# Optimization experiments

Hardware: AMD Instinct MI355X
Metric: run time of the kernel (lower is better)

The kernel has to match this reference:

```python
import jax, jax.numpy as jnp
import numpy as np

N_CELLS = 1024
HID = 256
IN_DIM = 256
OUT_DIM = 256
NOISE_DIM = 32
N_LOOP = 32  # min(32, n_cells)


def _lin(x, W, b):
    # torch nn.Linear: y = x @ W.T + b, W shape [out, in]
    return x @ W.T + b


def faction_sync_debate(h, step, n_factions=8, sync=0.15, debate=0.15):
    n, d = h.shape
    n_f = min(n_factions, n // 2)
    if n_f < 2:
        return h
    fs = n // n_f  # assumes n_f * fs == n (true for 1024/8)
    blk = h.reshape(n_f, fs, d)
    # per-faction mean pull (disjoint slices -> order independent)
    blk = (1.0 - sync) * blk + sync * blk.mean(axis=1, keepdims=True)
    if step > 5:  # step is a Python int -> static branch
        global_opinion = blk.mean(axis=1).mean(axis=0)  # [d]
        dc = max(1, fs // 4)
        blk = blk.at[:, :dc, :].set((1.0 - debate) * blk[:, :dc, :] + debate * global_opinion)
    return blk.reshape(n, d)


def setup_inputs() -> dict:
    key = jax.random.key(0)
    ks = iter(jax.random.split(key, 32))

    def rn(shape, scale=0.02):
        return (jax.random.normal(next(ks), shape, dtype=jnp.float32) * scale)

    flat = N_CELLS * HID  # 262144
    inp = {
        "x": rn((1, IN_DIM), 1.0),
        "noise": rn((1, NOISE_DIM), 1.0),
        "cell_hiddens": rn((N_CELLS, HID), 0.1),
        # generator: Linear(in+32,256) -> ReLU -> Linear(256,512) -> ReLU -> Linear(512, flat)
        "gen_W1": rn((256, IN_DIM + NOISE_DIM)), "gen_b1": rn((256,)),
        "gen_W2": rn((512, 256)), "gen_b2": rn((512,)),
        "gen_W3": rn((flat, 512)), "gen_b3": rn((flat,)),
        # discriminator: Linear(flat,512) -> LReLU(0.2) -> Linear(512,256) -> LReLU -> Linear(256,1) -> Sigmoid
        "disc_W1": rn((512, flat)), "disc_b1": rn((512,)),
        "disc_W2": rn((256, 512)), "disc_b2": rn((256,)),
        "disc_W3": rn((1, 256)), "disc_b3": rn((1,)),
        # mind engines: Linear(in+hid,128) -> ReLU -> Linear(128,out)
        "ea_W1": rn((128, IN_DIM + HID)), "ea_b1": rn((128,)),
        "ea_W2": rn((OUT_DIM, 128)), "ea_b2": rn((OUT_DIM,)),
        "eg_W1": rn((128, IN_DIM + HID)), "eg_b1": rn((128,)),
        "eg_W2": rn((OUT_DIM, 128)), "eg_b2": rn((OUT_DIM,)),
        # GRUCell(out+1, hid): gate order r, z, n
        "gru_Wih": rn((3 * HID, OUT_DIM + 1)), "gru_bih": rn((3 * HID,)),
        "gru_Whh": rn((3 * HID, HID)), "gru_bhh": rn((3 * HID,)),
        "step": 10,
    }
    return inp


def reference(x, noise, cell_hiddens,
              gen_W1, gen_b1, gen_W2, gen_b2, gen_W3, gen_b3,
              disc_W1, disc_b1, disc_W2, disc_b2, disc_W3, disc_b3,
              ea_W1, ea_b1, ea_W2, ea_b2, eg_W1, eg_b1, eg_W2, eg_b2,
              gru_Wih, gru_bih, gru_Whh, gru_bhh, step):
    sg = jax.lax.stop_gradient
    # --- generate_states ---
    gi = jnp.concatenate([x, noise], axis=-1)           # [1, in+32]
    h1 = jax.nn.relu(_lin(gi, gen_W1, gen_b1))
    h2 = jax.nn.relu(_lin(h1, gen_W2, gen_b2))
    gen_states = _lin(h2, gen_W3, gen_b3).reshape(N_CELLS, HID)
    # torch: gen_states.detach() then faction sync+debate
    synced = faction_sync_debate(sg(gen_states), step)
    # --- batched BenchMind over first 32 cells (replaces Python loop) ---
    H = synced[:N_LOOP]                                  # [32, HID]
    X = jnp.broadcast_to(x, (N_LOOP, x.shape[-1]))       # [32, IN]
    comb = jnp.concatenate([X, H], axis=-1)              # [32, IN+HID]
    a = _lin(jax.nn.relu(_lin(comb, ea_W1, ea_b1)), ea_W2, ea_b2)
    g = _lin(jax.nn.relu(_lin(comb, eg_W1, eg_b1)), eg_W2, eg_b2)
    outputs = a - g                                      # [32, OUT]
    tensions = (outputs ** 2).mean(axis=-1)              # [32]
    # GRUCell update (mem inputs detached as in torch)
    mem_in = jnp.concatenate([sg(outputs), sg(tensions)[:, None]], axis=-1)  # [32, OUT+1]
    gih = _lin(mem_in, gru_Wih, gru_bih)
    ghh = _lin(H, gru_Whh, gru_bhh)
    ir, iz, i_n = jnp.split(gih, 3, axis=-1)
    hr, hz, h_n = jnp.split(ghh, 3, axis=-1)
    r = jax.nn.sigmoid(ir + hr)
    z = jax.nn.sigmoid(iz + hz)
    n_cand = jnp.tanh(i_n + r * h_n)
    new_hiddens = (1.0 - z) * n_cand + z * H             # [32, HID]
    # --- buffer update (no_grad) + discriminate ---
    new_cell_hiddens = sg(0.7 * synced + 0.3 * cell_hiddens)

    def disc(s):
        f = s.reshape(1, -1)
        d1 = jax.nn.leaky_relu(_lin(f, disc_W1, disc_b1), 0.2)
        d2 = jax.nn.leaky_relu(_lin(d1, disc_W2, disc_b2), 0.2)
        return jax.nn.sigmoid(_lin(d2, disc_W3, disc_b3))

    d_real = disc(new_cell_hiddens)
    d_fake = disc(gen_states)
    # tensions were .item()'d in torch -> constants
    mean_tension = sg(tensions).mean()
    w = jax.nn.softmax(sg(tensions))                     # [32]
    combined = (w[:, None] * outputs).sum(axis=0, keepdims=True)  # [1, OUT]
    return combined, mean_tension, d_real, d_fake, new_hiddens
```

## Files before the change

kernel.cpp:

```cpp
#include <hip/hip_runtime.h>
#include <hip/hip_bf16.h>
#include <math.h>

#define N_CELLS 1024
#define HID     256
#define IN_DIM  256
#define NOISE_DIM 32
#define OUT_DIM 256
#define N_LOOP  32
#define FLAT    (N_CELLS*HID)

__device__ __forceinline__ float wave_reduce64(float v) {
    #pragma unroll
    for (int m = 32; m; m >>= 1) v += __shfl_xor(v, m);
    return v;
}
__device__ __forceinline__ float wave_reduce32(float v) {
    #pragma unroll
    for (int m = 16; m; m >>= 1) v += __shfl_xor(v, m);
    return v;
}

__global__ void k_gen_h1(const float* __restrict__ x, const float* __restrict__ noise,
                         const float* __restrict__ W1, const float* __restrict__ b1,
                         float* __restrict__ h1) {
    __shared__ __align__(16) float gi[288];
    int t = threadIdx.x, l = t & 63, w = t >> 6;
    gi[t] = x[t];
    if (t < 32) gi[256 + t] = noise[t];
    __syncthreads();
    int j = blockIdx.x * 4 + w;
    const float4* wr = (const float4*)(W1 + j * 288);
    const float4* g4 = (const float4*)gi;
    float4 a = wr[l], v = g4[l];
    float acc = a.x*v.x + a.y*v.y + a.z*v.z + a.w*v.w;
    if (l < 8) {
        float4 a2 = wr[64 + l], v2 = g4[64 + l];
        acc += a2.x*v2.x + a2.y*v2.y + a2.z*v2.z + a2.w*v2.w;
    }
    acc = wave_reduce64(acc);
    if (l == 0) h1[j] = fmaxf(acc + b1[j], 0.f);
}

__global__ void k_gen_h2(const float* __restrict__ h1, const float* __restrict__ W2,
                         const float* __restrict__ b2, float* __restrict__ h2) {
    int t = threadIdx.x, l = t & 63, w = t >> 6;
    int j = blockIdx.x * 4 + w;
    float4 a = ((const float4*)(W2 + j * 256))[l];
    float4 v = ((const float4*)h1)[l];
    float acc = a.x*v.x + a.y*v.y + a.z*v.z + a.w*v.w;
    acc = wave_reduce64(acc);
    if (l == 0) h2[j] = fmaxf(acc + b2[j], 0.f);
}

__global__ void k_gen_big(const float* __restrict__ W3, const float* __restrict__ b3,
                          const float* __restrict__ h2, float* __restrict__ gs) {
    int lane = threadIdx.x & 63;
    int row  = blockIdx.x * (blockDim.x >> 6) + (threadIdx.x >> 6);
    const float4* h24 = (const float4*)h2;
    float4 ha = h24[lane], hb = h24[64 + lane];
    const float4* w4 = (const float4*)(W3 + (size_t)row * 512);
    float4 wa = w4[lane], wb = w4[64 + lane];
    float acc = wa.x*ha.x + wa.y*ha.y + wa.z*ha.z + wa.w*ha.w
              + wb.x*hb.x + wb.y*hb.y + wb.z*hb.z + wb.w*hb.w;
    acc = wave_reduce64(acc);
    if (lane == 0) gs[row] = acc + b3[row];
}

__global__ void k_fmean(const float* __restrict__ gs, float* __restrict__ fmean) {
    __shared__ float part[4][64];
    int b = blockIdx.x, t = threadIdx.x;
    int f = b >> 2, q = b & 3;
    int c = q * 64 + (t & 63), rg = t >> 6;
    const float* base = gs + (size_t)(f * 128 + rg * 32) * 256 + c;
    float s = 0.f;
    for (int i = 0; i < 32; ++i) s += base[(size_t)i * 256];
    part[rg][t & 63] = s;
    __syncthreads();
    if (t < 64) {
        float v = part[0][t] + part[1][t] + part[2][t] + part[3][t];
        fmean[f * 256 + q * 64 + t] = v * (1.f / 128.f);
    }
}

__global__ void k_sync(const float* __restrict__ gs, const float* __restrict__ fmean,
                       const float* __restrict__ ch, const int* __restrict__ step,
                       const float* __restrict__ x,
                       float* __restrict__ synced, float* __restrict__ ncn,
                       float* __restrict__ comb) {
    int c = blockIdx.x, d = threadIdx.x;
    int f = c >> 7;
    float gm = 0.f;
    #pragma unroll
    for (int k = 0; k < 8; ++k) gm += fmean[k * 256 + d];
    gm *= 0.125f;
    float fm = fmean[f * 256 + d];
    float v = 0.85f * gs[c * 256 + d] + 0.15f * fm;
    if (((c & 127) < 32) && (*step > 5)) v = 0.85f * v + 0.15f * gm;
    synced[c * 256 + d] = v;
    ncn[c * 256 + d] = 0.7f * v + 0.3f * ch[c * 256 + d];
    if (c < N_LOOP) {
        comb[c * 512 + d] = x[d];
        comb[c * 512 + 256 + d] = v;
    }
}

__global__ void k_ev1(const float* __restrict__ comb,
                      const float* __restrict__ eaW1, const float* __restrict__ eab1,
                      const float* __restrict__ egW1, const float* __restrict__ egb1,
                      float* __restrict__ h1ag) {
    __shared__ __align__(16) float cl[N_LOOP * 512];
    int t = threadIdx.x, l = t & 63, w = t >> 6;
    const float4* cg = (const float4*)comb;
    float4* c4 = (float4*)cl;
    for (int i = t; i < N_LOOP * 128; i += 256) c4[i] = cg[i];
    __syncthreads();
    int j = blockIdx.x * 4 + w;
    const float* W = (j < 128) ? (eaW1 + j * 512) : (egW1 + (j - 128) * 512);
    float bias = (j < 128) ? eab1[j] : egb1[j - 128];
    const float4* w4 = (const float4*)W;
    float4 wa = w4[l], wb = w4[64 + l];
    for (int i = 0; i < N_LOOP; ++i) {
        const float4* ci = (const float4*)(cl + i * 512);
        float4 va = ci[l], vb = ci[64 + l];
        float acc = wa.x*va.x + wa.y*va.y + wa.z*va.z + wa.w*va.w
                  + wb.x*vb.x + wb.y*vb.y + wb.z*vb.z + wb.w*vb.w;
        acc = wave_reduce64(acc);
        if (l == 0) h1ag[i * 256 + j] = fmaxf(acc + bias, 0.f);
    }
}

__global__ void k_ev2(const float* __restrict__ h1ag,
                      const float* __restrict__ eaW2, const float* __restrict__ eab2,
                      const float* __restrict__ egW2, const float* __restrict__ egb2,
                      float* __restrict__ outputs) {
    __shared__ __align__(16) float hl[N_LOOP * 256];
    int t = threadIdx.x, l = t & 63, w = t >> 6;
    const float4* hg4 = (const float4*)h1ag;
    float4* h4 = (float4*)hl;
    for (int i = t; i < N_LOOP * 64; i += 256) h4[i] = hg4[i];
    __syncthreads();
    int half = l >> 5, sl = l & 31;
    int tr = (blockIdx.x * 4 + w) * 2 + half;
    float4 wa = ((const float4*)(eaW2 + tr * 128))[sl];
    float4 wg = ((const float4*)(egW2 + tr * 128))[sl];
    float bias = eab2[tr] - egb2[tr];
    for (int i = 0; i < N_LOOP; ++i) {
        float4 va = *(const float4*)(hl + i * 256 + sl * 4);
        float4 vg = *(const float4*)(hl + i * 256 + 128 + sl * 4);
        float acc = wa.x*va.x + wa.y*va.y + wa.z*va.z + wa.w*va.w
                  - (wg.x*vg.x + wg.y*vg.y + wg.z*vg.z + wg.w*vg.w);
        acc = wave_reduce32(acc);
        if (sl == 0) outputs[i * 256 + tr] = acc + bias;
    }
}

__global__ void k_tension(const float* __restrict__ outputs, float* __restrict__ tensions) {
    __shared__ float red[256];
    int i = blockIdx.x, t = threadIdx.x;
    float o = outputs[i * 256 + t];
    red[t] = o * o;
    __syncthreads();
    for (int m = 128; m; m >>= 1) { if (t < m) red[t] += red[t + m]; __syncthreads(); }
    if (t == 0) tensions[i] = red[0] * (1.f / 256.f);
}

__global__ void k_gru(const float* __restrict__ outputs, const float* __restrict__ tensions,
                      const float* __restrict__ synced,
                      const float* __restrict__ Wih, const float* __restrict__ bih,
                      const float* __restrict__ Whh, const float* __restrict__ bhh,
                      float* __restrict__ rz, float* __restrict__ inb, float* __restrict__ hnb) {
    __shared__ __align__(16) float outs[N_LOOP * 256];
    __shared__ __align__(16) float Hl[N_LOOP * 256];
    __shared__ float tl[N_LOOP];
    int t = threadIdx.x, l = t & 63, w = t >> 6;
    {
        const float4* o4 = (const float4*)outputs;
        const float4* s4 = (const float4*)synced;
        float4* od = (float4*)outs;
        float4* hd = (float4*)Hl;
        for (int i = t; i < N_LOOP * 64; i += 256) { od[i] = o4[i]; hd[i] = s4[i]; }
        if (t < N_LOOP) tl[t] = tensions[t];
    }
    __syncthreads();
    int u = blockIdx.x * 4 + w;
    const float* wr = Wih + (size_t)u * 257;
    float w0 = wr[4*l], w1 = wr[4*l+1], w2 = wr[4*l+2], w3 = wr[4*l+3];
    float wlast = wr[256];
    float4 wh = ((const float4*)(Whh + (size_t)u * 256))[l];
    float bg = bih[u], bh = bhh[u];
    bool isN = (u >= 512);
    for (int i = 0; i < N_LOOP; ++i) {
        const float* oi = outs + i * 256 + 4 * l;
        const float* hi = Hl + i * 256 + 4 * l;
        float ga = w0*oi[0] + w1*oi[1] + w2*oi[2] + w3*oi[3];
        float hh = wh.x*hi[0] + wh.y*hi[1] + wh.z*hi[2] + wh.w*hi[3];
        if (!isN) {
            float s = wave_reduce64(ga + hh);
            if (l == 0) rz[i * 512 + u] = s + bg + bh + wlast * tl[i];
        } else {
            float sg = wave_reduce64(ga);
            float sh = wave_reduce64(hh);
            if (l == 0) {
                inb[i * 256 + (u - 512)] = sg + bg + wlast * tl[i];
                hnb[i * 256 + (u - 512)] = sh + bh;
            }
        }
    }
}

__global__ void k_gru_fin(const float* __restrict__ rz, const float* __restrict__ inb,
                          const float* __restrict__ hnb, const float* __restrict__ synced,
                          float* __restrict__ out) {
    int i = blockIdx.x, d = threadIdx.x;
    float r = 1.f / (1.f + expf(-rz[i * 512 + d]));
    float z = 1.f / (1.f + expf(-rz[i * 512 + 256 + d]));
    float nc = tanhf(inb[i * 256 + d] + r * hnb[i * 256 + d]);
    float H = synced[i * 256 + d];
    out[259 + i * 256 + d] = (1.f - z) * nc + z * H;
}

__global__ void k_disc1(const float* __restrict__ W1, const float* __restrict__ b1,
                        const float* __restrict__ real, const float* __restrict__ fake,
                        float* __restrict__ d1r, float* __restrict__ d1f) {
    __shared__ float sR[1024];
    __shared__ float sF[1024];
    int row = blockIdx.x, t = threadIdx.x;
    const float4* w4 = (const float4*)(W1 + (size_t)row * FLAT);
    const float4* r4 = (const float4*)real;
    const float4* f4 = (const float4*)fake;
    float aR = 0.f, aF = 0.f;
    for (int i = t; i < FLAT / 4; i += 1024) {
        float4 w = w4[i], r = r4[i], f = f4[i];
        aR += w.x*r.x + w.y*r.y + w.z*r.z + w.w*r.w;
        aF += w.x*f.x + w.y*f.y + w.z*f.z + w.w*f.w;
    }
    sR[t] = aR; sF[t] = aF;
    __syncthreads();
    for (int m = 512; m; m >>= 1) {
        if (t < m) { sR[t] += sR[t + m]; sF[t] += sF[t + m]; }
        __syncthreads();
    }
    if (t == 0) { d1r[row] = sR[0] + b1[row]; d1f[row] = sF[0] + b1[row]; }
}

__global__ void k_disc_tail(const float* __restrict__ W2, const float* __restrict__ b2,
                            const float* __restrict__ W3, const float* __restrict__ b3,
                            const float* __restrict__ d1r, const float* __restrict__ d1f,
                            float* __restrict__ out) {
    __shared__ __align__(16) float lv[512];
    __shared__ float l2[256];
    __shared__ float red[256];
    int b = blockIdx.x, t = threadIdx.x;
    const float* d1 = b ? d1f : d1r;
    for (int j = t; j < 512; j += 256) { float v = d1[j]; lv[j] = v > 0.f ? v : 0.2f * v; }
    __syncthreads();
    {
        float acc = b2[t];
        const float4* wr = (const float4*)(W2 + t * 512);
        const float4* l4 = (const float4*)lv;
        for (int k = 0; k < 128; ++k) {
            float4 w = wr[k], v = l4[k];
            acc += w.x*v.x + w.y*v.y + w.z*v.z + w.w*v.w;
        }
        l2[t] = acc > 0.f ? acc : 0.2f * acc;
    }
    __syncthreads();
    red[t] = l2[t] * W3[t];
    __syncthreads();
    for (int m = 128; m; m >>= 1) { if (t < m) red[t] += red[t + m]; __syncthreads(); }
    if (t == 0) { float v = red[0] + b3[0]; out[257 + b] = 1.f / (1.f + expf(-v)); }
}

__global__ void k_combine(const float* __restrict__ outputs, const float* __restrict__ tensions,
                          float* __restrict__ out) {
    __shared__ float w[32];
    __shared__ float ts[32];
    int t = threadIdx.x;
    if (t < 32) ts[t] = tensions[t];
    __syncthreads();
    if (t == 0) {
        float mx = ts[0];
        for (int i = 1; i < 32; ++i) mx = fmaxf(mx, ts[i]);
        float s = 0.f, mean = 0.f;
        for (int i = 0; i < 32; ++i) { float e = expf(ts[i] - mx); w[i] = e; s += e; mean += ts[i]; }
        float inv = 1.f / s;
        for (int i = 0; i < 32; ++i) w[i] *= inv;
        out[256] = mean * (1.f / 32.f);
    }
    __syncthreads();
    float c = 0.f;
    for (int i = 0; i < 32; ++i) c += w[i] * outputs[i * 256 + t];
    out[t] = c;
}

extern "C" void kernel_launch(void* const* d_in, const int* in_sizes, int n_in,
                              void* d_out, int out_size, void* d_ws, size_t ws_size,
                              hipStream_t stream) {
    const float* x     = (const float*)d_in[0];
    const float* noise = (const float*)d_in[1];
    const float* ch    = (const float*)d_in[2];
    const float* gW1   = (const float*)d_in[3];
    const float* gb1   = (const float*)d_in[4];
    const float* gW2   = (const float*)d_in[5];
    const float* gb2   = (const float*)d_in[6];
    const float* gW3   = (const float*)d_in[7];
    const float* gb3   = (const float*)d_in[8];
    const float* dW1   = (const float*)d_in[9];
    const float* db1   = (const float*)d_in[10];
    const float* dW2   = (const float*)d_in[11];
    const float* db2   = (const float*)d_in[12];
    const float* dW3   = (const float*)d_in[13];
    const float* db3   = (const float*)d_in[14];
    const float* eaW1  = (const float*)d_in[15];
    const float* eab1  = (const float*)d_in[16];
    const float* eaW2  = (const float*)d_in[17];
    const float* eab2  = (const float*)d_in[18];
    const float* egW1  = (const float*)d_in[19];
    const float* egb1  = (const float*)d_in[20];
    const float* egW2  = (const float*)d_in[21];
    const float* egb2  = (const float*)d_in[22];
    const float* Wih   = (const float*)d_in[23];
    const float* bih   = (const float*)d_in[24];
    const float* Whh   = (const float*)d_in[25];
    const float* bhh   = (const float*)d_in[26];
    const int*   step  = (const int*)d_in[27];

    float* out = (float*)d_out;
    float* ws  = (float*)d_ws;
    float* h1buf    = ws;
    float* h2       = h1buf + 256;
    float* gs       = h2 + 512;
    float* fmean    = gs + 262144;
    float* synced   = fmean + 2048;
    float* ncn      = synced + 262144;
    float* comb     = ncn + 262144;
    float* h1ag     = comb + 16384;
    float* outputs  = h1ag + 8192;
    float* tensions = outputs + 8192;
    float* rz       = tensions + 32;
    float* inb      = rz + 16384;
    float* hnb      = inb + 8192;
    float* d1r      = hnb + 8192;
    float* d1f      = d1r + 512;

    k_gen_h1<<<64, 256, 0, stream>>>(x, noise, gW1, gb1, h1buf);
    k_gen_h2<<<128, 256, 0, stream>>>(h1buf, gW2, gb2, h2);
    k_gen_big<<<FLAT / 4, 256, 0, stream>>>(gW3, gb3, h2, gs);
    k_fmean<<<32, 256, 0, stream>>>(gs, fmean);
    k_sync<<<1024, 256, 0, stream>>>(gs, fmean, ch, step, x, synced, ncn, comb);
    k_ev1<<<64, 256, 0, stream>>>(comb, eaW1, eab1, egW1, egb1, h1ag);
    k_ev2<<<32, 256, 0, stream>>>(h1ag, eaW2, eab2, egW2, egb2, outputs);
    k_tension<<<32, 256, 0, stream>>>(outputs, tensions);
    k_gru<<<192, 256, 0, stream>>>(outputs, tensions, synced, Wih, bih, Whh, bhh, rz, inb, hnb);
    k_gru_fin<<<32, 256, 0, stream>>>(rz, inb, hnb, synced, out);
    k_disc1<<<512, 1024, 0, stream>>>(dW1, db1, ncn, gs, d1r, d1f);
    k_disc_tail<<<2, 256, 0, stream>>>(dW2, db2, dW3, db3, d1r, d1f, out);
    k_combine<<<1, 256, 0, stream>>>(outputs, tensions, out);
}
```

Before: 302.5 us.

## Fuse small post-generator stages into cooperative megakernel with grid syncs

Merges the generator head layers into one cooperative kernel, and fuses fmean, sync, both evaluator layers, tension, GRU, GRU finalisation and combine into a single cooperative kernel separated by grid-wide barriers. The goal is to remove many small kernel launches and their gaps, which dominate these tiny stages. It also rewrites the disc1 block reduction to use wave shuffles instead of a 1024-entry shared-memory tree. Shared-memory staging is dropped in favour of direct global/L2 reads, and the old kernels are kept as a fallback if the cooperative launch fails. Grid syncs carry their own cost and require all 512 blocks to be co-resident.

```diff
diff --git a/kernel.cpp b/kernel.cpp
--- a/kernel.cpp
+++ b/kernel.cpp
@@ -1,6 +1,8 @@
 #include <hip/hip_runtime.h>
-#include <hip/hip_bf16.h>
+#include <hip/hip_cooperative_groups.h>
 #include <math.h>
+
+namespace cg = cooperative_groups;
 
 #define N_CELLS 1024
 #define HID     256
@@ -21,36 +23,40 @@
     return v;
 }
 
-__global__ void k_gen_h1(const float* __restrict__ x, const float* __restrict__ noise,
-                         const float* __restrict__ W1, const float* __restrict__ b1,
-                         float* __restrict__ h1) {
+__global__ void __launch_bounds__(256)
+k_gen_head(const float* __restrict__ x, const float* __restrict__ noise,
+           const float* __restrict__ W1, const float* __restrict__ b1,
+           const float* __restrict__ W2, const float* __restrict__ b2,
+           float* __restrict__ h1, float* __restrict__ h2) {
+    cg::grid_group grid = cg::this_grid();
     __shared__ __align__(16) float gi[288];
     int t = threadIdx.x, l = t & 63, w = t >> 6;
-    gi[t] = x[t];
-    if (t < 32) gi[256 + t] = noise[t];
-    __syncthreads();
-    int j = blockIdx.x * 4 + w;
-    const float4* wr = (const float4*)(W1 + j * 288);
-    const float4* g4 = (const float4*)gi;
-    float4 a = wr[l], v = g4[l];
-    float acc = a.x*v.x + a.y*v.y + a.z*v.z + a.w*v.w;
-    if (l < 8) {
-        float4 a2 = wr[64 + l], v2 = g4[64 + l];
-        acc += a2.x*v2.x + a2.y*v2.y + a2.z*v2.z + a2.w*v2.w;
-    }
-    acc = wave_reduce64(acc);
-    if (l == 0) h1[j] = fmaxf(acc + b1[j], 0.f);
-}
-
-__global__ void k_gen_h2(const float* __restrict__ h1, const float* __restrict__ W2,
-                         const float* __restrict__ b2, float* __restrict__ h2) {
-    int t = threadIdx.x, l = t & 63, w = t >> 6;
-    int j = blockIdx.x * 4 + w;
-    float4 a = ((const float4*)(W2 + j * 256))[l];
-    float4 v = ((const float4*)h1)[l];
-    float acc = a.x*v.x + a.y*v.y + a.z*v.z + a.w*v.w;
-    acc = wave_reduce64(acc);
-    if (l == 0) h2[j] = fmaxf(acc + b2[j], 0.f);
+    int wid = blockIdx.x * 4 + w;
+    if (blockIdx.x < 64) {
+        gi[t] = x[t];
+        if (t < 32) gi[256 + t] = noise[t];
+        __syncthreads();
+        int j = wid;
+        const float4* wr = (const float4*)(W1 + j * 288);
+        const float4* g4 = (const float4*)gi;
+        float4 a = wr[l], v = g4[l];
+        float acc = a.x*v.x + a.y*v.y + a.z*v.z + a.w*v.w;
+        if (l < 8) {
+            float4 a2 = wr[64 + l], v2 = g4[64 + l];
+            acc += a2.x*v2.x + a2.y*v2.y + a2.z*v2.z + a2.w*v2.w;
+        }
+        acc = wave_reduce64(acc);
+        if (l == 0) h1[j] = fmaxf(acc + b1[j], 0.f);
+    }
+    grid.sync();
+    {
+        int j = wid;
+        float4 a = ((const float4*)(W2 + j * 256))[l];
+        float4 v = ((const float4*)h1)[l];
+        float acc = a.x*v.x + a.y*v.y + a.z*v.z + a.w*v.w;
+        acc = wave_reduce64(acc);
+        if (l == 0) h2[j] = fmaxf(acc + b2[j], 0.f);
+    }
 }
 
 __global__ void k_gen_big(const float* __restrict__ W3, const float* __restrict__ b3,
@@ -65,6 +71,248 @@
               + wb.x*hb.x + wb.y*hb.y + wb.z*hb.z + wb.w*hb.w;
     acc = wave_reduce64(acc);
     if (lane == 0) gs[row] = acc + b3[row];
+}
+
+__global__ void __launch_bounds__(256)
+k_mega(const float* __restrict__ gs, const float* __restrict__ ch,
+       const int* __restrict__ step, const float* __restrict__ x,
+       const float* __restrict__ eaW1, const float* __restrict__ eab1,
+       const float* __restrict__ eaW2, const float* __restrict__ eab2,
+       const float* __restrict__ egW1, const float* __restrict__ egb1,
+       const float* __restrict__ egW2, const float* __restrict__ egb2,
+       const float* __restrict__ Wih, const float* __restrict__ bih,
+       const float* __restrict__ Whh, const float* __restrict__ bhh,
+       float* __restrict__ fmean, float* __restrict__ synced,
+       float* __restrict__ ncn, float* __restrict__ comb,
+       float* __restrict__ h1ag, float* __restrict__ outputs,
+       float* __restrict__ tensions, float* __restrict__ rz,
+       float* __restrict__ inb, float* __restrict__ hnb,
+       float* __restrict__ out) {
+    cg::grid_group grid = cg::this_grid();
+    int b = blockIdx.x, t = threadIdx.x, l = t & 63, w = t >> 6;
+    __shared__ float s0[4][64];
+    __shared__ float red[256];
+    __shared__ float sw[32];
+    __shared__ float sts[32];
+
+    if (b < 32) {
+        int f = b >> 2, q = b & 3;
+        int c = q * 64 + l, rg = w;
+        const float* base = gs + (size_t)(f * 128 + rg * 32) * 256 + c;
+        float s = 0.f;
+        for (int i = 0; i < 32; ++i) s += base[(size_t)i * 256];
+        s0[rg][l] = s;
+        __syncthreads();
+        if (t < 64)
+            fmean[f * 256 + q * 64 + t] =
+                (s0[0][t] + s0[1][t] + s0[2][t] + s0[3][t]) * (1.f / 128.f);
+    }
+    grid.sync();
+
+    {
+        int d = t;
+        float gm = 0.f;
+        #pragma unroll
+        for (int k = 0; k < 8; ++k) gm += fmean[k * 256 + d];
+        gm *= 0.125f;
+        bool deb = (*step > 5);
+        #pragma unroll
+        for (int cc = 0; cc < 2; ++cc) {
+            int c = b * 2 + cc;
+            int f = c >> 7;
+            float fm = fmean[f * 256 + d];
+            float v = 0.85f * gs[c * 256 + d] + 0.15f * fm;
+            if (((c & 127) < 32) && deb) v = 0.85f * v + 0.15f * gm;
+            synced[c * 256 + d] = v;
+            ncn[c * 256 + d] = 0.7f * v + 0.3f * ch[c * 256 + d];
+            if (c < N_LOOP) { comb[c * 512 + d] = x[d]; comb[c * 512 + 256 + d] = v; }
+        }
+    }
+    grid.sync();
+
+    if (b < 64) {
+        int j = b * 4 + w;
+        const float* W = (j < 128) ? (eaW1 + j * 512) : (egW1 + (j - 128) * 512);
+        float bias = (j < 128) ? eab1[j] : egb1[j - 128];
+        const float4* w4 = (const float4*)W;
+        float4 wa = w4[l], wb = w4[64 + l];
+        for (int i = 0; i < N_LOOP; ++i) {
+            const float4* ci = (const float4*)(comb + i * 512);
+            float4 va = ci[l], vb = ci[64 + l];
+            float acc = wa.x*va.x + wa.y*va.y + wa.z*va.z + wa.w*va.w
+                      + wb.x*vb.x + wb.y*vb.y + wb.z*vb.z + wb.w*vb.w;
+            acc = wave_reduce64(acc);
+            if (l == 0) h1ag[i * 256 + j] = fmaxf(acc + bias, 0.f);
+        }
+    }
+    grid.sync();
+
+    if (b < 64) {
+        int tr = b * 4 + w;
+        bool lo = (l < 32);
+        int sl = l & 31;
+        float4 wv = lo ? ((const float4*)(eaW2 + tr * 128))[sl]
+                       : ((const float4*)(egW2 + tr * 128))[sl];
+        float bias = eab2[tr] - egb2[tr];
+        for (int i = 0; i < N_LOOP; ++i) {
+            const float* hrow = h1ag + i * 256 + (lo ? 0 : 128);
+            float4 v = *(const float4*)(hrow + sl * 4);
+            float d_ = wv.x*v.x + wv.y*v.y + wv.z*v.z + wv.w*v.w;
+            float acc = lo ? d_ : -d_;
+            acc = wave_reduce64(acc);
+            if (l == 0) outputs[i * 256 + tr] = acc + bias;
+        }
+    }
+    grid.sync();
+
+    if (b < 32) {
+        float o = outputs[b * 256 + t];
+        red[t] = o * o;
+        __syncthreads();
+        for (int m = 128; m; m >>= 1) { if (t < m) red[t] += red[t + m]; __syncthreads(); }
+        if (t == 0) tensions[b] = red[0] * (1.f / 256.f);
+    }
+    grid.sync();
+
+    if (b < 192) {
+        int u = b * 4 + w;
+        const float* wr = Wih + (size_t)u * 257;
+        float w0 = wr[4*l], w1 = wr[4*l+1], w2 = wr[4*l+2], w3 = wr[4*l+3];
+        float wlast = wr[256];
+        float4 wh = ((const float4*)(Whh + (size_t)u * 256))[l];
+        float bg = bih[u], bh = bhh[u];
+        bool isN = (u >= 512);
+        for (int i = 0; i < N_LOOP; ++i) {
+            const float* oi = outputs + i * 256 + 4 * l;
+            const float* hi = synced + i * 256 + 4 * l;
+            float ga = w0*oi[0] + w1*oi[1] + w2*oi[2] + w3*oi[3];
+            float hh = wh.x*hi[0] + wh.y*hi[1] + wh.z*hi[2] + wh.w*hi[3];
+            if (!isN) {
+                float s = wave_reduce64(ga + hh);
+                if (l == 0) rz[i * 512 + u] = s + bg + bh + wlast * tensions[i];
+            } else {
+                float sg2 = wave_reduce64(ga);
+                float sh  = wave_reduce64(hh);
+                if (l == 0) {
+                    inb[i * 256 + (u - 512)] = sg2 + bg + wlast * tensions[i];
+                    hnb[i * 256 + (u - 512)] = sh + bh;
+                }
+            }
+        }
+    }
+    grid.sync();
+
+    if (b < 32) {
+        int i = b, d = t;
+        float r = 1.f / (1.f + expf(-rz[i * 512 + d]));
+        float z = 1.f / (1.f + expf(-rz[i * 512 + 256 + d]));
+        float nc = tanhf(inb[i * 256 + d] + r * hnb[i * 256 + d]);
+        float H = synced[i * 256 + d];
+        out[259 + i * 256 + d] = (1.f - z) * nc + z * H;
+    } else if (b == 32) {
+        if (t < 32) sts[t] = tensions[t];
+        __syncthreads();
+        if (t == 0) {
+            float mx = sts[0];
+            for (int i2 = 1; i2 < 32; ++i2) mx = fmaxf(mx, sts[i2]);
+            float s = 0.f, mean = 0.f;
+            for (int i2 = 0; i2 < 32; ++i2) { float e = expf(sts[i2] - mx); sw[i2] = e; s += e; mean += sts[i2]; }
+            float inv = 1.f / s;
+            for (int i2 = 0; i2 < 32; ++i2) sw[i2] *= inv;
+            out[256] = mean * (1.f / 32.f);
+        }
+        __syncthreads();
+        float c = 0.f;
+        for (int i2 = 0; i2 < 32; ++i2) c += sw[i2] * outputs[i2 * 256 + t];
+        out[t] = c;
+    }
+}
+
+__global__ void k_disc1(const float* __restrict__ W1, const float* __restrict__ b1,
+                        const float* __restrict__ real, const float* __restrict__ fake,
+                        float* __restrict__ d1r, float* __restrict__ d1f) {
+    __shared__ float sR[16];
+    __shared__ float sF[16];
+    int row = blockIdx.x, t = threadIdx.x, l = t & 63, w = t >> 6;
+    const float4* w4 = (const float4*)(W1 + (size_t)row * FLAT);
+    const float4* r4 = (const float4*)real;
+    const float4* f4 = (const float4*)fake;
+    float aR = 0.f, aF = 0.f;
+    for (int i = t; i < FLAT / 4; i += 1024) {
+        float4 ww = w4[i], r = r4[i], f = f4[i];
+        aR += ww.x*r.x + ww.y*r.y + ww.z*r.z + ww.w*r.w;
+        aF += ww.x*f.x + ww.y*f.y + ww.z*f.z + ww.w*f.w;
+    }
+    aR = wave_reduce64(aR);
+    aF = wave_reduce64(aF);
+    if (l == 0) { sR[w] = aR; sF[w] = aF; }
+    __syncthreads();
+    if (t < 16) {
+        float r = sR[t], f = sF[t];
+        #pragma unroll
+        for (int m = 8; m; m >>= 1) { r += __shfl_xor(r, m); f += __shfl_xor(f, m); }
+        if (t == 0) { d1r[row] = r + b1[row]; d1f[row] = f + b1[row]; }
+    }
+}
+
+__global__ void k_disc_tail(const float* __restrict__ W2, const float* __restrict__ b2,
+                            const float* __restrict__ W3, const float* __restrict__ b3,
+                            const float* __restrict__ d1r, const float* __restrict__ d1f,
+                            float* __restrict__ out) {
+    __shared__ __align__(16) float lv[512];
+    __shared__ float l2[256];
+    __shared__ float red[256];
+    int b = blockIdx.x, t = threadIdx.x;
+    const float* d1 = b ? d1f : d1r;
+    for (int j = t; j < 512; j += 256) { float v = d1[j]; lv[j] = v > 0.f ? v : 0.2f * v; }
+    __syncthreads();
+    {
+        float acc = b2[t];
+        const float4* wr = (const float4*)(W2 + t * 512);
+        const float4* l4 = (const float4*)lv;
+        for (int k = 0; k < 128; ++k) {
+            float4 w = wr[k], v = l4[k];
+            acc += w.x*v.x + w.y*v.y + w.z*v.z + w.w*v.w;
+        }
+        l2[t] = acc > 0.f ? acc : 0.2f * acc;
+    }
+    __syncthreads();
+    red[t] = l2[t] * W3[t];
+    __syncthreads();
+    for (int m = 128; m; m >>= 1) { if (t < m) red[t] += red[t + m]; __syncthreads(); }
+    if (t == 0) { float v = red[0] + b3[0]; out[257 + b] = 1.f / (1.f + expf(-v)); }
+}
+
+__global__ void k_gen_h1(const float* __restrict__ x, const float* __restrict__ noise,
+                         const float* __restrict__ W1, const float* __restrict__ b1,
+                         float* __restrict__ h1) {
+    __shared__ __align__(16) float gi[288];
+    int t = threadIdx.x, l = t & 63, w = t >> 6;
+    gi[t] = x[t];
+    if (t < 32) gi[256 + t] = noise[t];
+    __syncthreads();
+    int j = blockIdx.x * 4 + w;
+    const float4* wr = (const float4*)(W1 + j * 288);
+    const float4* g4 = (const float4*)gi;
+    float4 a = wr[l], v = g4[l];
+    float acc = a.x*v.x + a.y*v.y + a.z*v.z + a.w*v.w;
+    if (l < 8) {
+        float4 a2 = wr[64 + l], v2 = g4[64 + l];
+        acc += a2.x*v2.x + a2.y*v2.y + a2.z*v2.z + a2.w*v2.w;
+    }
+    acc = wave_reduce64(acc);
+    if (l == 0) h1[j] = fmaxf(acc + b1[j], 0.f);
+}
+
+__global__ void k_gen_h2(const float* __restrict__ h1, const float* __restrict__ W2,
+                         const float* __restrict__ b2, float* __restrict__ h2) {
+    int t = threadIdx.x, l = t & 63, w = t >> 6;
+    int j = blockIdx.x * 4 + w;
+    float4 a = ((const float4*)(W2 + j * 256))[l];
+    float4 v = ((const float4*)h1)[l];
+    float acc = a.x*v.x + a.y*v.y + a.z*v.z + a.w*v.w;
+    acc = wave_reduce64(acc);
+    if (l == 0) h2[j] = fmaxf(acc + b2[j], 0.f);
 }
 
 __global__ void k_fmean(const float* __restrict__ gs, float* __restrict__ fmean) {
@@ -109,19 +357,14 @@
                       const float* __restrict__ eaW1, const float* __restrict__ eab1,
                       const float* __restrict__ egW1, const float* __restrict__ egb1,
                       float* __restrict__ h1ag) {
-    __shared__ __align__(16) float cl[N_LOOP * 512];
     int t = threadIdx.x, l = t & 63, w = t >> 6;
-    const float4* cg = (const float4*)comb;
-    float4* c4 = (float4*)cl;
-    for (int i = t; i < N_LOOP * 128; i += 256) c4[i] = cg[i];
-    __syncthreads();
     int j = blockIdx.x * 4 + w;
     const float* W = (j < 128) ? (eaW1 + j * 512) : (egW1 + (j - 128) * 512);
     float bias = (j < 128) ? eab1[j] : egb1[j - 128];
     const float4* w4 = (const float4*)W;
     float4 wa = w4[l], wb = w4[64 + l];
     for (int i = 0; i < N_LOOP; ++i) {
-        const float4* ci = (const float4*)(cl + i * 512);
+        const float4* ci = (const float4*)(comb + i * 512);
         float4 va = ci[l], vb = ci[64 + l];
         float acc = wa.x*va.x + wa.y*va.y + wa.z*va.z + wa.w*va.w
                   + wb.x*vb.x + wb.y*vb.y + wb.z*vb.z + wb.w*vb.w;
@@ -134,24 +377,20 @@
                       const float* __restrict__ eaW2, const float* __restrict__ eab2,
                       const float* __restrict__ egW2, const float* __restrict__ egb2,
                       float* __restrict__ outputs) {
-    __shared__ __align__(16) float hl[N_LOOP * 256];
     int t = threadIdx.x, l = t & 63, w = t >> 6;
-    const float4* hg4 = (const float4*)h1ag;
-    float4* h4 = (float4*)hl;
-    for (int i = t; i < N_LOOP * 64; i += 256) h4[i] = hg4[i];
-    __syncthreads();
-    int half = l >> 5, sl = l & 31;
-    int tr = (blockIdx.x * 4 + w) * 2 + half;
-    float4 wa = ((const float4*)(eaW2 + tr * 128))[sl];
-    float4 wg = ((const float4*)(egW2 + tr * 128))[sl];
+    int tr = blockIdx.x * 4 + w;
+    bool lo = (l < 32);
+    int sl = l & 31;
+    float4 wv = lo ? ((const float4*)(eaW2 + tr * 128))[sl]
+                   : ((const float4*)(egW2 + tr * 128))[sl];
     float bias = eab2[tr] - egb2[tr];
     for (int i = 0; i < N_LOOP; ++i) {
-        float4 va = *(const float4*)(hl + i * 256 + sl * 4);
-        float4 vg = *(const float4*)(hl + i * 256 + 128 + sl * 4);
-        float acc = wa.x*va.x + wa.y*va.y + wa.z*va.z + wa.w*va.w
-                  - (wg.x*vg.x + wg.y*vg.y + wg.z*vg.z + wg.w*vg.w);
-        acc = wave_reduce32(acc);
-        if (sl == 0) outputs[i * 256 + tr] = acc + bias;
+        const float* hrow = h1ag + i * 256 + (lo ? 0 : 128);
+        float4 v = *(const float4*)(hrow + sl * 4);
+        float d_ = wv.x*v.x + wv.y*v.y + wv.z*v.z + wv.w*v.w;
+        float acc = lo ? d_ : -d_;
+        acc = wave_reduce64(acc);
+        if (l == 0) outputs[i * 256 + tr] = acc + bias;
     }
 }
 
@@ -170,19 +409,7 @@
                       const float* __restrict__ Wih, const float* __restrict__ bih,
                       const float* __restrict__ Whh, const float* __restrict__ bhh,
                       float* __restrict__ rz, float* __restrict__ inb, float* __restrict__ hnb) {
-    __shared__ __align__(16) float outs[N_LOOP * 256];
-    __shared__ __align__(16) float Hl[N_LOOP * 256];
-    __shared__ float tl[N_LOOP];
     int t = threadIdx.x, l = t & 63, w = t >> 6;
-    {
-        const float4* o4 = (const float4*)outputs;
-        const float4* s4 = (const float4*)synced;
-        float4* od = (float4*)outs;
-        float4* hd = (float4*)Hl;
-        for (int i = t; i < N_LOOP * 64; i += 256) { od[i] = o4[i]; hd[i] = s4[i]; }
-        if (t < N_LOOP) tl[t] = tensions[t];
-    }
-    __syncthreads();
     int u = blockIdx.x * 4 + w;
     const float* wr = Wih + (size_t)u * 257;
     float w0 = wr[4*l], w1 = wr[4*l+1], w2 = wr[4*l+2], w3 = wr[4*l+3];
@@ -191,18 +418,18 @@
     float bg = bih[u], bh = bhh[u];
     bool isN = (u >= 512);
     for (int i = 0; i < N_LOOP; ++i) {
-        const float* oi = outs + i * 256 + 4 * l;
-        const float* hi = Hl + i * 256 + 4 * l;
+        const float* oi = outputs + i * 256 + 4 * l;
+        const float* hi = synced + i * 256 + 4 * l;
         float ga = w0*oi[0] + w1*oi[1] + w2*oi[2] + w3*oi[3];
         float hh = wh.x*hi[0] + wh.y*hi[1] + wh.z*hi[2] + wh.w*hi[3];
         if (!isN) {
             float s = wave_reduce64(ga + hh);
-            if (l == 0) rz[i * 512 + u] = s + bg + bh + wlast * tl[i];
+            if (l == 0) rz[i * 512 + u] = s + bg + bh + wlast * tensions[i];
         } else {
-            float sg = wave_reduce64(ga);
-            float sh = wave_reduce64(hh);
+            float sg2 = wave_reduce64(ga);
+            float sh  = wave_reduce64(hh);
             if (l == 0) {
-                inb[i * 256 + (u - 512)] = sg + bg + wlast * tl[i];
+                inb[i * 256 + (u - 512)] = sg2 + bg + wlast * tensions[i];
                 hnb[i * 256 + (u - 512)] = sh + bh;
             }
         }
@@ -218,58 +445,6 @@
     float nc = tanhf(inb[i * 256 + d] + r * hnb[i * 256 + d]);
     float H = synced[i * 256 + d];
     out[259 + i * 256 + d] = (1.f - z) * nc + z * H;
-}
-
-__global__ void k_disc1(const float* __restrict__ W1, const float* __restrict__ b1,
-                        const float* __restrict__ real, const float* __restrict__ fake,
-                        float* __restrict__ d1r, float* __restrict__ d1f) {
-    __shared__ float sR[1024];
-    __shared__ float sF[1024];
-    int row = blockIdx.x, t = threadIdx.x;
-    const float4* w4 = (const float4*)(W1 + (size_t)row * FLAT);
-    const float4* r4 = (const float4*)real;
-    const float4* f4 = (const float4*)fake;
-    float aR = 0.f, aF = 0.f;
-    for (int i = t; i < FLAT / 4; i += 1024) {
-        float4 w = w4[i], r = r4[i], f = f4[i];
-        aR += w.x*r.x + w.y*r.y + w.z*r.z + w.w*r.w;
-        aF += w.x*f.x + w.y*f.y + w.z*f.z + w.w*f.w;
-    }
-    sR[t] = aR; sF[t] = aF;
-    __syncthreads();
-    for (int m = 512; m; m >>= 1) {
-        if (t < m) { sR[t] += sR[t + m]; sF[t] += sF[t + m]; }
-        __syncthreads();
-    }
-    if (t == 0) { d1r[row] = sR[0] + b1[row]; d1f[row] = sF[0] + b1[row]; }
-}
-
-__global__ void k_disc_tail(const float* __restrict__ W2, const float* __restrict__ b2,
-                            const float* __restrict__ W3, const float* __restrict__ b3,
-                            const float* __restrict__ d1r, const float* __restrict__ d1f,
-                            float* __restrict__ out) {
-    __shared__ __align__(16) float lv[512];
-    __shared__ float l2[256];
-    __shared__ float red[256];
-    int b = blockIdx.x, t = threadIdx.x;
-    const float* d1 = b ? d1f : d1r;
-    for (int j = t; j < 512; j += 256) { float v = d1[j]; lv[j] = v > 0.f ? v : 0.2f * v; }
-    __syncthreads();
-    {
-        float acc = b2[t];
-        const float4* wr = (const float4*)(W2 + t * 512);
-        const float4* l4 = (const float4*)lv;
-        for (int k = 0; k < 128; ++k) {
-            float4 w = wr[k], v = l4[k];
-            acc += w.x*v.x + w.y*v.y + w.z*v.z + w.w*v.w;
-        }
-        l2[t] = acc > 0.f ? acc : 0.2f * acc;
-    }
-    __syncthreads();
-    red[t] = l2[t] * W3[t];
-    __syncthreads();
-    for (int m = 128; m; m >>= 1) { if (t < m) red[t] += red[t + m]; __syncthreads(); }
-    if (t == 0) { float v = red[0] + b3[0]; out[257 + b] = 1.f / (1.f + expf(-v)); }
 }
 
 __global__ void k_combine(const float* __restrict__ outputs, const float* __restrict__ tensions,
@@ -344,17 +519,41 @@
     float* d1r      = hnb + 8192;
     float* d1f      = d1r + 512;
 
-    k_gen_h1<<<64, 256, 0, stream>>>(x, noise, gW1, gb1, h1buf);
-    k_gen_h2<<<128, 256, 0, stream>>>(h1buf, gW2, gb2, h2);
+    {
+        void* a[] = {(void*)&x, (void*)&noise, (void*)&gW1, (void*)&gb1,
+                     (void*)&gW2, (void*)&gb2, (void*)&h1buf, (void*)&h2};
+        hipError_t e = hipLaunchCooperativeKernel((const void*)k_gen_head,
+                                                  dim3(128), dim3(256), a, 0, stream);
+        if (e != hipSuccess) {
+            k_gen_h1<<<64, 256, 0, stream>>>(x, noise, gW1, gb1, h1buf);
+            k_gen_h2<<<128, 256, 0, stream>>>(h1buf, gW2, gb2, h2);
+        }
+    }
+
     k_gen_big<<<FLAT / 4, 256, 0, stream>>>(gW3, gb3, h2, gs);
-    k_fmean<<<32, 256, 0, stream>>>(gs, fmean);
-    k_sync<<<1024, 256, 0, stream>>>(gs, fmean, ch, step, x, synced, ncn, comb);
-    k_ev1<<<64, 256, 0, stream>>>(comb, eaW1, eab1, egW1, egb1, h1ag);
-    k_ev2<<<32, 256, 0, stream>>>(h1ag, eaW2, eab2, egW2, egb2, outputs);
-    k_tension<<<32, 256, 0, stream>>>(outputs, tensions);
-    k_gru<<<192, 256, 0, stream>>>(outputs, tensions, synced, Wih, bih, Whh, bhh, rz, inb, hnb);
-    k_gru_fin<<<32, 256, 0, stream>>>(rz, inb, hnb, synced, out);
+
+    {
+        void* a[] = {(void*)&gs, (void*)&ch, (void*)&step, (void*)&x,
+                     (void*)&eaW1, (void*)&eab1, (void*)&eaW2, (void*)&eab2,
+                     (void*)&egW1, (void*)&egb1, (void*)&egW2, (void*)&egb2,
+                     (void*)&Wih, (void*)&bih, (void*)&Whh, (void*)&bhh,
+                     (void*)&fmean, (void*)&synced, (void*)&ncn, (void*)&comb,
+                     (void*)&h1ag, (void*)&outputs, (void*)&tensions,
+                     (void*)&rz, (void*)&inb, (void*)&hnb, (void*)&out};
+        hipError_t e = hipLaunchCooperativeKernel((const void*)k_mega,
+                                                  dim3(512), dim3(256), a, 0, stream);
+        if (e != hipSuccess) {
+            k_fmean<<<32, 256, 0, stream>>>(gs, fmean);
+            k_sync<<<1024, 256, 0, stream>>>(gs, fmean, ch, step, x, synced, ncn, comb);
+            k_ev1<<<64, 256, 0, stream>>>(comb, eaW1, eab1, egW1, egb1, h1ag);
+            k_ev2<<<64, 256, 0, stream>>>(h1ag, eaW2, eab2, egW2, egb2, outputs);
+            k_tension<<<32, 256, 0, stream>>>(outputs, tensions);
+            k_gru<<<192, 256, 0, stream>>>(outputs, tensions, synced, Wih, bih, Whh, bhh, rz, inb, hnb);
+            k_gru_fin<<<32, 256, 0, stream>>>(rz, inb, hnb, synced, out);
+            k_combine<<<1, 256, 0, stream>>>(outputs, tensions, out);
+        }
+    }
+
     k_disc1<<<512, 1024, 0, stream>>>(dW1, db1, ncn, gs, d1r, d1f);
     k_disc_tail<<<2, 256, 0, stream>>>(dW2, db2, dW3, db3, d1r, d1f, out);
-    k_combine<<<1, 256, 0, stream>>>(outputs, tensions, out);
-}
+}
```

Result: slower. 654.9 us (+116.5%).
